# Kernel optimization log

Hardware: AMD Instinct MI355X
Metric: run time of the kernel (lower is better)

Reference implementation:

```python
import jax, jax.numpy as jnp
import numpy as np

N, D, H, L, T, R = 50000, 128, 8, 2, 4, 8
E = 800000
HD = D // H  # head_size = 16
SQRT_D = float(np.sqrt(HD))


def typed_linear(x, types, W):
    # x: (n, Din), types: (n,), W: (T, Din, Dout)  -- per-type dense projection
    out = jnp.zeros((x.shape[0], W.shape[-1]), x.dtype)
    for t in range(W.shape[0]):
        out = out + jnp.where((types == t)[:, None], x @ W[t], 0.0)
    return out


def rel_typed(x, etype, W):
    # x: (E, H, d), etype: (E,), W: (H, R, d, d) -- per-head, per-edge-type linear
    out = jnp.zeros_like(x)
    for r in range(W.shape[1]):
        out = out + jnp.where((etype == r)[:, None, None], jnp.einsum('ehd,hdo->eho', x, W[:, r]), 0.0)
    return out


def edge_softmax(a, dst, n):
    # softmax over incoming edges per destination node, per head. a: (E, H)
    amax = jax.ops.segment_max(a, dst, num_segments=n)
    amax = jnp.where(jnp.isfinite(amax), amax, 0.0)
    ex = jnp.exp(a - amax[dst])
    s = jax.ops.segment_sum(ex, dst, num_segments=n)
    return ex / (s[dst] + 1e-9)


def layer_norm(x, g, b, eps=1e-5):
    mu = x.mean(-1, keepdims=True)
    var = ((x - mu) ** 2).mean(-1, keepdims=True)
    return (x - mu) * jax.lax.rsqrt(var + eps) * g + b


def hgt_conv(x, ntype, etype, src, dst, Wk, Wq, Wv, Wa, ratt, rmsg, rpri, skip):
    n = x.shape[0]
    k = typed_linear(x, ntype, Wk).reshape(n, H, HD)
    q = typed_linear(x, ntype, Wq).reshape(n, H, HD)
    v = typed_linear(x, ntype, Wv).reshape(n, H, HD)
    kw = rel_typed(k[src], etype, ratt)               # (E, H, d)
    pri = rpri[:, etype].T                            # (E, H)
    a = (kw * q[dst]).sum(-1) * pri / SQRT_D          # (E, H)
    m = rel_typed(v[src], etype, rmsg)                # (E, H, d)
    att = edge_softmax(a, dst, n)                     # (E, H)
    h = jax.ops.segment_sum(m * att[..., None], dst, num_segments=n)
    h = h.reshape(n, D)
    h = typed_linear(h, ntype, Wa)                    # dropout off (eval)
    alpha = jax.nn.sigmoid(skip[ntype])[:, None]
    return h * alpha + x * (1.0 - alpha)


def setup_inputs() -> dict:
    key = jax.random.key(0)
    ks = jax.random.split(key, 12)
    g_lin = float(np.sqrt(2.0 / (D + D)))   # xavier-ish scale for D x D
    g_rel = float(np.sqrt(2.0 / (HD + HD)))
    g_emb = float(np.sqrt(2.0 / (N + D)))
    return {
        'embed': jax.random.normal(ks[0], (T, N, D), jnp.float32) * g_emb,
        'Wk': jax.random.normal(ks[1], (L, T, D, D), jnp.float32) * g_lin,
        'Wq': jax.random.normal(ks[2], (L, T, D, D), jnp.float32) * g_lin,
        'Wv': jax.random.normal(ks[3], (L, T, D, D), jnp.float32) * g_lin,
        'Wa': jax.random.normal(ks[4], (L, T, D, D), jnp.float32) * g_lin,
        'rel_att': jax.random.normal(ks[5], (L, H, R, HD, HD), jnp.float32) * g_rel,
        'rel_msg': jax.random.normal(ks[6], (L, H, R, HD, HD), jnp.float32) * g_rel,
        'rel_pri': jnp.ones((L, H, R), jnp.float32),
        'skip': jnp.ones((L, T), jnp.float32),
        'ln_g': jnp.ones((L, D), jnp.float32),
        'ln_b': jnp.zeros((L, D), jnp.float32),
        'src': jax.random.randint(ks[7], (E,), 0, N, jnp.int32),
        'dst': jax.random.randint(ks[8], (E,), 0, N, jnp.int32),
        'ntype': jax.random.randint(ks[9], (N,), 0, T, jnp.int32),
        'etype': jax.random.randint(ks[10], (E,), 0, R, jnp.int32),
    }


def reference(embed, Wk, Wq, Wv, Wa, rel_att, rel_msg, rel_pri, skip, ln_g, ln_b, src, dst, ntype, etype):
    # masked per-type embedding init: node gets row <rank-within-its-type> of its type table
    onehot = jax.nn.one_hot(ntype, T, dtype=jnp.int32)
    rank = jnp.take_along_axis(jnp.cumsum(onehot, axis=0), ntype[:, None], axis=1)[:, 0] - 1
    h = embed[ntype, rank]                            # (N, D)
    for l in range(L):
        h_prev = h
        hc = hgt_conv(h, ntype, etype, src, dst,
                      Wk[l], Wq[l], Wv[l], Wa[l],
                      rel_att[l], rel_msg[l], rel_pri[l], skip[l])
        h = layer_norm(hc, ln_g[l], ln_b[l]) + h_prev
    return h
```

## Files before the change

kernel.cpp:

```cpp
#include <hip/hip_runtime.h>
#include <math.h>

#define N_NODES 50000
#define DIM     128
#define NHEAD   8
#define HDIM    16
#define NLAYER  2
#define NTYPE   4
#define NREL    8
#define NEDGE   800000
#define RB      256
#define GN      8
#define NK      (N_NODES * NREL)

__device__ __forceinline__ float blo(unsigned w) { return __uint_as_float(w << 16); }
__device__ __forceinline__ float bhi(unsigned w) { return __uint_as_float(w & 0xFFFF0000u); }
__device__ __forceinline__ unsigned short f2bf(float f) {
    unsigned b = __float_as_uint(f);
    b += 0x7FFFu + ((b >> 16) & 1u);
    return (unsigned short)(b >> 16);
}


__global__ void k_hist(const int* __restrict__ ntype, int* __restrict__ hist, int n) {
    __shared__ int cnt[NTYPE];
    if (threadIdx.x < NTYPE) cnt[threadIdx.x] = 0;
    __syncthreads();
    int i = blockIdx.x * RB + threadIdx.x;
    if (i < n) atomicAdd(&cnt[ntype[i]], 1);
    __syncthreads();
    if (threadIdx.x < NTYPE) hist[blockIdx.x * NTYPE + threadIdx.x] = cnt[threadIdx.x];
}

__global__ void k_prefix(const int* __restrict__ hist, int* __restrict__ off, int nb) {
    int t = threadIdx.x;
    if (t >= NTYPE) return;
    int acc = 0;
    for (int b = 0; b < nb; b++) { off[b * NTYPE + t] = acc; acc += hist[b * NTYPE + t]; }
}

__global__ void k_rank(const int* __restrict__ ntype, const int* __restrict__ off,
                       int* __restrict__ rank, int n) {
    __shared__ int ty[RB];
    int i = blockIdx.x * RB + threadIdx.x;
    int t = (i < n) ? ntype[i] : -1;
    ty[threadIdx.x] = t;
    __syncthreads();
    if (i < n) {
        int c = 0;
        for (int j = 0; j < (int)threadIdx.x; j++) c += (ty[j] == t);
        rank[i] = off[blockIdx.x * NTYPE + t] + c;
    }
}

__global__ void k_embed(const float* __restrict__ embed, const int* __restrict__ ntype,
                        const int* __restrict__ rank, float* __restrict__ h) {
    int i = blockIdx.x;
    int t = ntype[i], r = rank[i];
    h[(size_t)i * DIM + threadIdx.x] = embed[((size_t)t * N_NODES + r) * DIM + threadIdx.x];
}

__global__ void k_typeoff(const int* __restrict__ hist, const int* __restrict__ boff,
                          int nb, int* __restrict__ typeoff) {
    if (threadIdx.x == 0 && blockIdx.x == 0) {
        int acc = 0;
        for (int t = 0; t < NTYPE; t++) {
            typeoff[t] = acc;
            acc += boff[(nb - 1) * NTYPE + t] + hist[(nb - 1) * NTYPE + t];
        }
    }
}

__global__ void k_perm(const int* __restrict__ ntype, const int* __restrict__ rank,
                       const int* __restrict__ typeoff, int* __restrict__ perm, int n) {
    int i = blockIdx.x * 256 + threadIdx.x;
    if (i < n) perm[typeoff[ntype[i]] + rank[i]] = i;
}


__global__ void k_deg2(const int* __restrict__ dst, const int* __restrict__ etype,
                       int* __restrict__ deg) {
    int e = blockIdx.x * 256 + threadIdx.x;
    if (e < NEDGE) atomicAdd(&deg[dst[e] * NREL + etype[e]], 1);
}

__global__ void k_scan1(const int* __restrict__ deg, int* __restrict__ rs,
                        int* __restrict__ bsum, int n) {
    __shared__ int sh[256];
    int i = blockIdx.x * 256 + threadIdx.x;
    int v = (i < n) ? deg[i] : 0;
    sh[threadIdx.x] = v;
    __syncthreads();
    for (int off = 1; off < 256; off <<= 1) {
        int x = (threadIdx.x >= off) ? sh[threadIdx.x - off] : 0;
        __syncthreads();
        sh[threadIdx.x] += x;
        __syncthreads();
    }
    if (i < n) rs[i] = sh[threadIdx.x] - v;
    if (threadIdx.x == 255) bsum[blockIdx.x] = sh[255];
}

__global__ void k_scan2b(int* __restrict__ bsum, int nb) {
    __shared__ int sh[256];
    __shared__ int carry;
    if (threadIdx.x == 0) carry = 0;
    __syncthreads();
    for (int base = 0; base < nb; base += 256) {
        int i = base + threadIdx.x;
        int v = (i < nb) ? bsum[i] : 0;
        sh[threadIdx.x] = v;
        __syncthreads();
        for (int off = 1; off < 256; off <<= 1) {
            int x = (threadIdx.x >= off) ? sh[threadIdx.x - off] : 0;
            __syncthreads();
            sh[threadIdx.x] += x;
            __syncthreads();
        }
        if (i < nb) bsum[i] = sh[threadIdx.x] - v + carry;
        __syncthreads();
        if (threadIdx.x == 0) carry += sh[255];
        __syncthreads();
    }
}

__global__ void k_scan3(int* __restrict__ rs, const int* __restrict__ bsum, int n) {
    int i = blockIdx.x * 256 + threadIdx.x;
    if (i < n) rs[i] += bsum[blockIdx.x];
    if (i == 0) rs[n] = NEDGE;
}

__global__ void k_scatter2(const int* __restrict__ src, const int* __restrict__ dst,
                           const int* __restrict__ etype, const int* __restrict__ rs,
                           int* __restrict__ cur, int* __restrict__ epk) {
    int e = blockIdx.x * 256 + threadIdx.x;
    if (e < NEDGE) {
        int et = etype[e];
        int key = dst[e] * NREL + et;
        int p = atomicAdd(&cur[key], 1);
        epk[rs[key] + p] = src[e] | (et << 24);
    }
}


__global__ void k_rmsgT(const float* __restrict__ rmsg, float* __restrict__ rmsgT) {
    int b = blockIdx.x;
    int d = threadIdx.x >> 4, o = threadIdx.x & 15;
    rmsgT[b * 256 + o * 16 + d] = rmsg[b * 256 + d * 16 + o];
}

__global__ void k_rattB(const float* __restrict__ ratt, unsigned short* __restrict__ rattB) {
    int i = blockIdx.x * 256 + threadIdx.x;
    rattB[i] = f2bf(ratt[i]);
}


__global__ __launch_bounds__(128) void k_qkvvt_g(
        const float* __restrict__ h, const int* __restrict__ perm, const int* __restrict__ ntype,
        const float* __restrict__ Wk, const float* __restrict__ Wq, const float* __restrict__ Wv,
        const float* __restrict__ rmsgT,
        unsigned short* __restrict__ kb, float* __restrict__ qout,
        unsigned short* __restrict__ vt, int n) {
    int o = threadIdx.x;
    int base = blockIdx.x * GN;
    __shared__ float xs[GN][DIM];
    __shared__ int nodes[GN];
    __shared__ int types[GN];
    if (o < GN) {
        int idx = base + o;
        int nd = (idx < n) ? perm[idx] : -1;
        nodes[o] = nd;
        types[o] = (nd >= 0) ? ntype[nd] : -1;
    }
    __syncthreads();
    #pragma unroll
    for (int nn = 0; nn < GN; nn++)
        if (nodes[nn] >= 0) xs[nn][o] = h[(size_t)nodes[nn] * DIM + o];
    __syncthreads();
    bool same = (nodes[GN - 1] >= 0) && (types[0] == types[GN - 1]);
    float av[GN];
    if (same) {
        int t = types[0];
        const float* wk = Wk + (size_t)t * DIM * DIM;
        const float* wq = Wq + (size_t)t * DIM * DIM;
        const float* wv = Wv + (size_t)t * DIM * DIM;
        float ak[GN], aq[GN];
        #pragma unroll
        for (int nn = 0; nn < GN; nn++) { ak[nn] = 0.f; aq[nn] = 0.f; av[nn] = 0.f; }
        for (int d = 0; d < DIM; d++) {
            float wkv = wk[d * DIM + o], wqv = wq[d * DIM + o], wvv = wv[d * DIM + o];
            #pragma unroll
            for (int nn = 0; nn < GN; nn++) {
                float xv = xs[nn][d];
                ak[nn] = fmaf(xv, wkv, ak[nn]);
                aq[nn] = fmaf(xv, wqv, aq[nn]);
                av[nn] = fmaf(xv, wvv, av[nn]);
            }
        }
        #pragma unroll
        for (int nn = 0; nn < GN; nn++) {
            size_t p = (size_t)nodes[nn] * DIM + o;
            kb[p] = f2bf(ak[nn]); qout[p] = aq[nn];
        }
    } else {
        #pragma unroll 1
        for (int nn = 0; nn < GN; nn++) {
            av[nn] = 0.f;
            if (nodes[nn] < 0) continue;
            int t = types[nn];
            const float* wk = Wk + (size_t)t * DIM * DIM;
            const float* wq = Wq + (size_t)t * DIM * DIM;
            const float* wv = Wv + (size_t)t * DIM * DIM;
            float ak = 0.f, aq = 0.f, avv = 0.f;
            for (int d = 0; d < DIM; d++) {
                float xv = xs[nn][d];
                ak = fmaf(xv, wk[d * DIM + o], ak);
                aq = fmaf(xv, wq[d * DIM + o], aq);
                avv = fmaf(xv, wv[d * DIM + o], avv);
            }
            size_t p = (size_t)nodes[nn] * DIM + o;
            kb[p] = f2bf(ak); qout[p] = aq;
            av[nn] = avv;
        }
    }
    __syncthreads();
    #pragma unroll
    for (int nn = 0; nn < GN; nn++) xs[nn][o] = av[nn];
    __syncthreads();
    int hh = o >> 4, oo = o & 15;
    #pragma unroll 1
    for (int et = 0; et < NREL; et++) {
        const float4* w4 = (const float4*)(rmsgT + ((size_t)(hh * NREL + et) * HDIM + oo) * HDIM);
        float4 w0 = w4[0], w1 = w4[1], w2 = w4[2], w3 = w4[3];
        #pragma unroll
        for (int nn = 0; nn < GN; nn++) {
            if (nodes[nn] < 0) continue;
            const float4* v4 = (const float4*)&xs[nn][hh * HDIM];
            float4 v0 = v4[0], v1 = v4[1], v2 = v4[2], v3 = v4[3];
            float acc = v0.x*w0.x + v0.y*w0.y + v0.z*w0.z + v0.w*w0.w
                      + v1.x*w1.x + v1.y*w1.y + v1.z*w1.z + v1.w*w1.w
                      + v2.x*w2.x + v2.y*w2.y + v2.z*w2.z + v2.w*w2.w
                      + v3.x*w3.x + v3.y*w3.y + v3.z*w3.z + v3.w*w3.w;
            vt[((size_t)nodes[nn] * NREL + et) * DIM + o] = f2bf(acc);
        }
    }
}


__global__ __launch_bounds__(128) void k_fused10(
        const unsigned short* __restrict__ kb, const float* __restrict__ qbuf,
        const unsigned short* __restrict__ vt,
        const int* __restrict__ rs2, const int* __restrict__ epk,
        const unsigned short* __restrict__ rattB, const float* __restrict__ rpri,
        float* __restrict__ agg) {
    int node = blockIdx.x;
    int tid = threadIdx.x;
    int hh = tid >> 4, oo = tid & 15;
    int wv = tid >> 6;
    int hl = hh & 3;

    __shared__ float q_s[DIM];
    __shared__ float u_s[NREL][NHEAD * HDIM + 4];
    __shared__ float a_sw[2][4][HDIM + 1];
    __shared__ int   es_sw[2][HDIM];

    int e0 = rs2[node * NREL];
    int e1 = rs2[node * NREL + NREL];
    if (e0 == e1) { agg[(size_t)node * DIM + tid] = 0.f; return; }

    q_s[tid] = qbuf[(size_t)node * DIM + tid];
    {
        const float4* q4 = (const float4*)&q_s[hh * HDIM];
        float4 q0 = q4[0], q1 = q4[1], q2 = q4[2], q3 = q4[3];
        #pragma unroll
        for (int et = 0; et < NREL; et++) {
            const uint4* wB = (const uint4*)(rattB + ((size_t)(hh * NREL + et) * HDIM + oo) * HDIM);
            uint4 wa = wB[0], wb = wB[1];
            float s = blo(wa.x)*q0.x + bhi(wa.x)*q0.y + blo(wa.y)*q0.z + bhi(wa.y)*q0.w
                    + blo(wa.z)*q1.x + bhi(wa.z)*q1.y + blo(wa.w)*q1.z + bhi(wa.w)*q1.w
                    + blo(wb.x)*q2.x + bhi(wb.x)*q2.y + blo(wb.y)*q2.z + bhi(wb.y)*q2.w
                    + blo(wb.z)*q3.x + bhi(wb.z)*q3.y + blo(wb.w)*q3.z + bhi(wb.w)*q3.w;
            u_s[et][tid] = s * rpri[hh * NREL + et] * 0.25f;
        }
    }

    float m_h = -1e30f, s_h = 0.f, out = 0.f;

    for (int w0e = e0; w0e < e1; w0e += HDIM) {
        int cnt = min(HDIM, e1 - w0e);
        float a = -1e30f;
        int pk = 0;
        if (oo < cnt) {
            pk = epk[w0e + oo];
            int sv = pk & 0x00FFFFFF;
            int et = ((unsigned)pk) >> 24;
            const uint4* kr = (const uint4*)(kb + (size_t)sv * DIM + hh * HDIM);
            uint4 ka = kr[0], kc = kr[1];
            const float4* u4 = (const float4*)&u_s[et][hh * HDIM];
            float4 u0 = u4[0], u1 = u4[1], u2 = u4[2], u3 = u4[3];
            a = blo(ka.x)*u0.x + bhi(ka.x)*u0.y + blo(ka.y)*u0.z + bhi(ka.y)*u0.w
              + blo(ka.z)*u1.x + bhi(ka.z)*u1.y + blo(ka.w)*u1.z + bhi(ka.w)*u1.w
              + blo(kc.x)*u2.x + bhi(kc.x)*u2.y + blo(kc.y)*u2.z + bhi(kc.y)*u2.w
              + blo(kc.z)*u3.x + bhi(kc.z)*u3.y + blo(kc.w)*u3.z + bhi(kc.w)*u3.w;
        }
        if (hl == 0) es_sw[wv][oo] = pk;
        float cmax = a;
        cmax = fmaxf(cmax, __shfl_xor(cmax, 1));
        cmax = fmaxf(cmax, __shfl_xor(cmax, 2));
        cmax = fmaxf(cmax, __shfl_xor(cmax, 4));
        cmax = fmaxf(cmax, __shfl_xor(cmax, 8));
        float m_t = (cmax > m_h + 12.f) ? cmax : m_h;
        float r = __expf(m_h - m_t);
        s_h *= r; out *= r; m_h = m_t;
        float p = (oo < cnt) ? __expf(a - m_h) : 0.f;
        float ps = p;
        ps += __shfl_xor(ps, 1);
        ps += __shfl_xor(ps, 2);
        ps += __shfl_xor(ps, 4);
        ps += __shfl_xor(ps, 8);
        s_h += ps;
        a_sw[wv][hl][oo] = p;
        for (int c = 0; c < cnt; c++) {
            float pc = a_sw[wv][hl][c];
            int pkc = es_sw[wv][c];
            int sv = pkc & 0x00FFFFFF;
            int et = ((unsigned)pkc) >> 24;
            unsigned short uv = vt[((size_t)sv * NREL + et) * DIM + tid];
            out = fmaf(pc, __uint_as_float((unsigned)uv << 16), out);
        }
    }

    agg[(size_t)node * DIM + tid] = out / (s_h + 1e-9f);
}


__global__ __launch_bounds__(128) void k_out_g(
        const float* __restrict__ agg, float* __restrict__ h,
        const int* __restrict__ perm, const int* __restrict__ ntype,
        const float* __restrict__ Wa, const float* __restrict__ skip,
        const float* __restrict__ ln_g, const float* __restrict__ ln_b, int n) {
    int o = threadIdx.x;
    int base = blockIdx.x * GN;
    __shared__ float xs[GN][DIM];
    __shared__ float hcs[GN][DIM + 1];
    __shared__ int nodes[GN];
    __shared__ int types[GN];
    __shared__ float mu_s[GN], rs_s[GN];
    if (o < GN) {
        int idx = base + o;
        int nd = (idx < n) ? perm[idx] : -1;
        nodes[o] = nd;
        types[o] = (nd >= 0) ? ntype[nd] : -1;
    }
    __syncthreads();
    #pragma unroll
    for (int nn = 0; nn < GN; nn++)
        if (nodes[nn] >= 0) xs[nn][o] = agg[(size_t)nodes[nn] * DIM + o];
    __syncthreads();
    bool same = (nodes[GN - 1] >= 0) && (types[0] == types[GN - 1]);
    if (same) {
        int t = types[0];
        const float* w = Wa + (size_t)t * DIM * DIM;
        float acc[GN];
        #pragma unroll
        for (int nn = 0; nn < GN; nn++) acc[nn] = 0.f;
        for (int d = 0; d < DIM; d++) {
            float wv = w[d * DIM + o];
            #pragma unroll
            for (int nn = 0; nn < GN; nn++) acc[nn] = fmaf(xs[nn][d], wv, acc[nn]);
        }
        float alpha = 1.f / (1.f + __expf(-skip[t]));
        #pragma unroll
        for (int nn = 0; nn < GN; nn++) {
            float hp = h[(size_t)nodes[nn] * DIM + o];
            hcs[nn][o] = acc[nn] * alpha + hp * (1.f - alpha);
        }
    } else {
        #pragma unroll 1
        for (int nn = 0; nn < GN; nn++) {
            if (nodes[nn] < 0) continue;
            int t = types[nn];
            const float* w = Wa + (size_t)t * DIM * DIM;
            float a0 = 0.f;
            for (int d = 0; d < DIM; d++) a0 = fmaf(xs[nn][d], w[d * DIM + o], a0);
            float alpha = 1.f / (1.f + __expf(-skip[t]));
            float hp = h[(size_t)nodes[nn] * DIM + o];
            hcs[nn][o] = a0 * alpha + hp * (1.f - alpha);
        }
    }
    __syncthreads();
    {
        int g = o >> 4, j = o & 15;
        if (nodes[g] >= 0) {
            float s = 0.f;
            for (int d = j; d < DIM; d += 16) s += hcs[g][d];
            #pragma unroll
            for (int m = 1; m < 16; m <<= 1) s += __shfl_xor(s, m);
            float mu = s * (1.f / DIM);
            float v = 0.f;
            for (int d = j; d < DIM; d += 16) { float dv = hcs[g][d] - mu; v = fmaf(dv, dv, v); }
            #pragma unroll
            for (int m = 1; m < 16; m <<= 1) v += __shfl_xor(v, m);
            if (j == 0) { mu_s[g] = mu; rs_s[g] = rsqrtf(v * (1.f / DIM) + 1e-5f); }
        }
    }
    __syncthreads();
    float g_o = ln_g[o], b_o = ln_b[o];
    #pragma unroll
    for (int nn = 0; nn < GN; nn++) {
        if (nodes[nn] >= 0) {
            float hp = h[(size_t)nodes[nn] * DIM + o];
            h[(size_t)nodes[nn] * DIM + o] = (hcs[nn][o] - mu_s[nn]) * rs_s[nn] * g_o + b_o + hp;
        }
    }
}


extern "C" void kernel_launch(void* const* d_in, const int* in_sizes, int n_in,
                              void* d_out, int out_size, void* d_ws, size_t ws_size,
                              hipStream_t stream) {
    const float* embed = (const float*)d_in[0];
    const float* Wk    = (const float*)d_in[1];
    const float* Wq    = (const float*)d_in[2];
    const float* Wv    = (const float*)d_in[3];
    const float* Wa    = (const float*)d_in[4];
    const float* ratt  = (const float*)d_in[5];
    const float* rmsg  = (const float*)d_in[6];
    const float* rpri  = (const float*)d_in[7];
    const float* skip  = (const float*)d_in[8];
    const float* ln_g  = (const float*)d_in[9];
    const float* ln_b  = (const float*)d_in[10];
    const int*   src   = (const int*)d_in[11];
    const int*   dst   = (const int*)d_in[12];
    const int*   ntype = (const int*)d_in[13];
    const int*   etype = (const int*)d_in[14];

    float* h = (float*)d_out;

    const size_t ND = (size_t)N_NODES * DIM;
    const int nb = (N_NODES + RB - 1) / RB;
    unsigned short* kb = (unsigned short*)d_ws;
    float* qbuf = (float*)(kb + ND);
    int* rs2  = (int*)(qbuf + ND);
    int* deg2 = rs2 + (NK + 1);
    int* cur2 = deg2 + NK;
    int* epk  = cur2 + NK;
    int* bsum = epk + NEDGE;
    int* rank = bsum + 2048;
    int* hist = rank + N_NODES;
    int* boff = hist + nb * NTYPE;
    int* typeoff = boff + nb * NTYPE;
    int* perm = typeoff + NTYPE;
    float* rmsgT = (float*)(perm + N_NODES);
    unsigned short* rattB = (unsigned short*)(rmsgT + (size_t)NLAYER * NHEAD * NREL * 256);
    unsigned short* vt = rattB + (size_t)NLAYER * NHEAD * NREL * 256;
    float* agg = qbuf;

    const int EB = (NEDGE + 255) / 256;
    const int nb2 = (NK + 255) / 256;

    k_hist<<<nb, RB, 0, stream>>>(ntype, hist, N_NODES);
    k_prefix<<<1, 64, 0, stream>>>(hist, boff, nb);
    k_rank<<<nb, RB, 0, stream>>>(ntype, boff, rank, N_NODES);
    k_embed<<<N_NODES, DIM, 0, stream>>>(embed, ntype, rank, h);
    k_typeoff<<<1, 64, 0, stream>>>(hist, boff, nb, typeoff);
    k_perm<<<nb, 256, 0, stream>>>(ntype, rank, typeoff, perm, N_NODES);

    hipMemsetAsync(deg2, 0, (size_t)NK * sizeof(int), stream);
    hipMemsetAsync(cur2, 0, (size_t)NK * sizeof(int), stream);
    k_deg2<<<EB, 256, 0, stream>>>(dst, etype, deg2);
    k_scan1<<<nb2, 256, 0, stream>>>(deg2, rs2, bsum, NK);
    k_scan2b<<<1, 256, 0, stream>>>(bsum, nb2);
    k_scan3<<<nb2, 256, 0, stream>>>(rs2, bsum, NK);
    k_scatter2<<<EB, 256, 0, stream>>>(src, dst, etype, rs2, cur2, epk);

    k_rmsgT<<<NLAYER * NHEAD * NREL, 256, 0, stream>>>(rmsg, rmsgT);
    k_rattB<<<NLAYER * NHEAD * NREL, 256, 0, stream>>>(ratt, rattB);

    const int NGB = N_NODES / GN;

    for (int l = 0; l < NLAYER; l++) {
        const float* Wk_l = Wk + (size_t)l * NTYPE * DIM * DIM;
        const float* Wq_l = Wq + (size_t)l * NTYPE * DIM * DIM;
        const float* Wv_l = Wv + (size_t)l * NTYPE * DIM * DIM;
        const float* Wa_l = Wa + (size_t)l * NTYPE * DIM * DIM;
        const unsigned short* rattB_l = rattB + (size_t)l * NHEAD * NREL * 256;
        const float* rmsgT_l = rmsgT + (size_t)l * NHEAD * NREL * 256;
        const float* rpri_l = rpri + (size_t)l * NHEAD * NREL;
        const float* skip_l = skip + (size_t)l * NTYPE;
        const float* g_l = ln_g + (size_t)l * DIM;
        const float* b_l = ln_b + (size_t)l * DIM;

        k_qkvvt_g<<<NGB, 128, 0, stream>>>(h, perm, ntype, Wk_l, Wq_l, Wv_l, rmsgT_l,
                                           kb, qbuf, vt, N_NODES);
        k_fused10<<<N_NODES, 128, 0, stream>>>(kb, qbuf, vt, rs2, epk,
                                               rattB_l, rpri_l, agg);
        k_out_g<<<NGB, 128, 0, stream>>>(agg, h, perm, ntype, Wa_l, skip_l, g_l, b_l, N_NODES);
    }
}
```

Baseline: 749.7 us.

## Compute typed QKV projections with bf16 MFMA on 32-node tiles

Replaces the scalar FP32 QKV projection kernel with one using bf16 MFMA 16x16x32 instructions over 32-node tiles of same-type nodes. The K, Q and V weights are pre-packed once into a bf16 fragment layout. Activations are converted to bf16 on load, which lowers precision of q and v. Mixed-type tiles fall back to a scalar path, and the V relation transform stays in FP32 from shared memory.

```diff
diff --git a/kernel.cpp b/kernel.cpp
--- a/kernel.cpp
+++ b/kernel.cpp
@@ -11,7 +11,11 @@
 #define NEDGE   800000
 #define RB      256
 #define GN      8
+#define MT      32
 #define NK      (N_NODES * NREL)
+
+typedef __attribute__((ext_vector_type(8))) short bf16x8;
+typedef __attribute__((ext_vector_type(4))) float f32x4;
 
 __device__ __forceinline__ float blo(unsigned w) { return __uint_as_float(w << 16); }
 __device__ __forceinline__ float bhi(unsigned w) { return __uint_as_float(w & 0xFFFF0000u); }
@@ -19,6 +23,14 @@
     unsigned b = __float_as_uint(f);
     b += 0x7FFFu + ((b >> 16) & 1u);
     return (unsigned short)(b >> 16);
+}
+__device__ __forceinline__ bf16x8 pack8(float4 x0, float4 x1) {
+    bf16x8 r;
+    r[0] = (short)f2bf(x0.x); r[1] = (short)f2bf(x0.y);
+    r[2] = (short)f2bf(x0.z); r[3] = (short)f2bf(x0.w);
+    r[4] = (short)f2bf(x1.x); r[5] = (short)f2bf(x1.y);
+    r[6] = (short)f2bf(x1.z); r[7] = (short)f2bf(x1.w);
+    return r;
 }
 
 
@@ -154,94 +166,134 @@
     rattB[i] = f2bf(ratt[i]);
 }
 
-
-__global__ __launch_bounds__(128) void k_qkvvt_g(
+__global__ void k_packW(const float* __restrict__ W, unsigned short* __restrict__ WB) {
+    int t = blockIdx.x;
+    const float* w = W + (size_t)t * 16384;
+    unsigned short* ob = WB + (size_t)t * 16384;
+    for (int idx = threadIdx.x; idx < 16384; idx += 256) {
+        int ct = idx >> 11, kc = (idx >> 9) & 3, l = (idx >> 3) & 63, j = idx & 7;
+        int k = kc * 32 + ((l >> 4) << 3) + j;
+        int c = ct * 16 + (l & 15);
+        ob[idx] = f2bf(w[k * 128 + c]);
+    }
+}
+
+
+__global__ __launch_bounds__(256) void k_qkv_mfma(
         const float* __restrict__ h, const int* __restrict__ perm, const int* __restrict__ ntype,
         const float* __restrict__ Wk, const float* __restrict__ Wq, const float* __restrict__ Wv,
-        const float* __restrict__ rmsgT,
+        const unsigned short* __restrict__ WkB, const unsigned short* __restrict__ WqB,
+        const unsigned short* __restrict__ WvB, const float* __restrict__ rmsgT,
         unsigned short* __restrict__ kb, float* __restrict__ qout,
         unsigned short* __restrict__ vt, int n) {
-    int o = threadIdx.x;
-    int base = blockIdx.x * GN;
-    __shared__ float xs[GN][DIM];
-    __shared__ int nodes[GN];
-    __shared__ int types[GN];
-    if (o < GN) {
-        int idx = base + o;
+    int tid = threadIdx.x;
+    int base = blockIdx.x * MT;
+    __shared__ int nodes_s[MT];
+    __shared__ int types_s[MT];
+    __shared__ float vs[MT][132];
+
+    if (tid < MT) {
+        int idx = base + tid;
         int nd = (idx < n) ? perm[idx] : -1;
-        nodes[o] = nd;
-        types[o] = (nd >= 0) ? ntype[nd] : -1;
-    }
-    __syncthreads();
-    #pragma unroll
-    for (int nn = 0; nn < GN; nn++)
-        if (nodes[nn] >= 0) xs[nn][o] = h[(size_t)nodes[nn] * DIM + o];
-    __syncthreads();
-    bool same = (nodes[GN - 1] >= 0) && (types[0] == types[GN - 1]);
-    float av[GN];
+        nodes_s[tid] = nd;
+        types_s[tid] = (nd >= 0) ? ntype[nd] : -1;
+    }
+    __syncthreads();
+    bool same = (nodes_s[MT - 1] >= 0) && (types_s[0] == types_s[MT - 1]);
+
     if (same) {
-        int t = types[0];
-        const float* wk = Wk + (size_t)t * DIM * DIM;
-        const float* wq = Wq + (size_t)t * DIM * DIM;
-        const float* wv = Wv + (size_t)t * DIM * DIM;
-        float ak[GN], aq[GN];
+        int l = tid & 63, w = tid >> 6;
+        int t = types_s[0];
+        const unsigned short* wbk = WkB + (size_t)t * 16384;
+        const unsigned short* wbq = WqB + (size_t)t * 16384;
+        const unsigned short* wbv = WvB + (size_t)t * 16384;
+        f32x4 acc[3][2][2];
         #pragma unroll
-        for (int nn = 0; nn < GN; nn++) { ak[nn] = 0.f; aq[nn] = 0.f; av[nn] = 0.f; }
-        for (int d = 0; d < DIM; d++) {
-            float wkv = wk[d * DIM + o], wqv = wq[d * DIM + o], wvv = wv[d * DIM + o];
+        for (int m = 0; m < 3; m++)
             #pragma unroll
-            for (int nn = 0; nn < GN; nn++) {
-                float xv = xs[nn][d];
-                ak[nn] = fmaf(xv, wkv, ak[nn]);
-                aq[nn] = fmaf(xv, wqv, aq[nn]);
-                av[nn] = fmaf(xv, wvv, av[nn]);
+            for (int a = 0; a < 2; a++)
+                #pragma unroll
+                for (int b = 0; b < 2; b++) {
+                    acc[m][a][b][0] = 0.f; acc[m][a][b][1] = 0.f;
+                    acc[m][a][b][2] = 0.f; acc[m][a][b][3] = 0.f;
+                }
+        #pragma unroll 1
+        for (int kc = 0; kc < 4; kc++) {
+            int koff = kc * 32 + ((l >> 4) << 3);
+            int r0 = l & 15;
+            const float4* p0 = (const float4*)(h + (size_t)nodes_s[r0] * DIM + koff);
+            bf16x8 a0 = pack8(p0[0], p0[1]);
+            const float4* p1 = (const float4*)(h + (size_t)nodes_s[16 + r0] * DIM + koff);
+            bf16x8 a1 = pack8(p1[0], p1[1]);
+            #pragma unroll
+            for (int cti = 0; cti < 2; cti++) {
+                int boff = ((w * 2 + cti) * 4 + kc) * 512 + l * 8;
+                bf16x8 bk = *(const bf16x8*)(wbk + boff);
+                acc[0][0][cti] = __builtin_amdgcn_mfma_f32_16x16x32_bf16(a0, bk, acc[0][0][cti], 0, 0, 0);
+                acc[0][1][cti] = __builtin_amdgcn_mfma_f32_16x16x32_bf16(a1, bk, acc[0][1][cti], 0, 0, 0);
+                bf16x8 bq = *(const bf16x8*)(wbq + boff);
+                acc[1][0][cti] = __builtin_amdgcn_mfma_f32_16x16x32_bf16(a0, bq, acc[1][0][cti], 0, 0, 0);
+                acc[1][1][cti] = __builtin_amdgcn_mfma_f32_16x16x32_bf16(a1, bq, acc[1][1][cti], 0, 0, 0);
+                bf16x8 bv = *(const bf16x8*)(wbv + boff);
+                acc[2][0][cti] = __builtin_amdgcn_mfma_f32_16x16x32_bf16(a0, bv, acc[2][0][cti], 0, 0, 0);
+                acc[2][1][cti] = __builtin_amdgcn_mfma_f32_16x16x32_bf16(a1, bv, acc[2][1][cti], 0, 0, 0);
             }
         }
         #pragma unroll
-        for (int nn = 0; nn < GN; nn++) {
-            size_t p = (size_t)nodes[nn] * DIM + o;
-            kb[p] = f2bf(ak[nn]); qout[p] = aq[nn];
-        }
+        for (int mt = 0; mt < 2; mt++)
+            #pragma unroll
+            for (int cti = 0; cti < 2; cti++) {
+                int col = w * 32 + cti * 16 + (l & 15);
+                #pragma unroll
+                for (int r = 0; r < 4; r++) {
+                    int row = mt * 16 + ((l >> 4) << 2) + r;
+                    size_t p = (size_t)nodes_s[row] * DIM + col;
+                    kb[p] = f2bf(acc[0][mt][cti][r]);
+                    qout[p] = acc[1][mt][cti][r];
+                    vs[row][col] = acc[2][mt][cti][r];
+                }
+            }
     } else {
-        #pragma unroll 1
-        for (int nn = 0; nn < GN; nn++) {
-            av[nn] = 0.f;
-            if (nodes[nn] < 0) continue;
-            int t = types[nn];
-            const float* wk = Wk + (size_t)t * DIM * DIM;
-            const float* wq = Wq + (size_t)t * DIM * DIM;
-            const float* wv = Wv + (size_t)t * DIM * DIM;
-            float ak = 0.f, aq = 0.f, avv = 0.f;
+        int o = tid & 127, half = tid >> 7;
+        for (int nn = half; nn < MT; nn += 2) {
+            int nd = nodes_s[nn];
+            if (nd < 0) continue;
+            int t = types_s[nn];
+            const float* wk = Wk + (size_t)t * 16384;
+            const float* wq = Wq + (size_t)t * 16384;
+            const float* wv = Wv + (size_t)t * 16384;
+            float ak = 0.f, aq = 0.f, av = 0.f;
             for (int d = 0; d < DIM; d++) {
-                float xv = xs[nn][d];
+                float xv = h[(size_t)nd * DIM + d];
                 ak = fmaf(xv, wk[d * DIM + o], ak);
                 aq = fmaf(xv, wq[d * DIM + o], aq);
-                avv = fmaf(xv, wv[d * DIM + o], avv);
+                av = fmaf(xv, wv[d * DIM + o], av);
             }
-            size_t p = (size_t)nodes[nn] * DIM + o;
+            size_t p = (size_t)nd * DIM + o;
             kb[p] = f2bf(ak); qout[p] = aq;
-            av[nn] = avv;
-        }
-    }
-    __syncthreads();
-    #pragma unroll
-    for (int nn = 0; nn < GN; nn++) xs[nn][o] = av[nn];
-    __syncthreads();
-    int hh = o >> 4, oo = o & 15;
-    #pragma unroll 1
-    for (int et = 0; et < NREL; et++) {
-        const float4* w4 = (const float4*)(rmsgT + ((size_t)(hh * NREL + et) * HDIM + oo) * HDIM);
-        float4 w0 = w4[0], w1 = w4[1], w2 = w4[2], w3 = w4[3];
-        #pragma unroll
-        for (int nn = 0; nn < GN; nn++) {
-            if (nodes[nn] < 0) continue;
-            const float4* v4 = (const float4*)&xs[nn][hh * HDIM];
-            float4 v0 = v4[0], v1 = v4[1], v2 = v4[2], v3 = v4[3];
-            float acc = v0.x*w0.x + v0.y*w0.y + v0.z*w0.z + v0.w*w0.w
-                      + v1.x*w1.x + v1.y*w1.y + v1.z*w1.z + v1.w*w1.w
-                      + v2.x*w2.x + v2.y*w2.y + v2.z*w2.z + v2.w*w2.w
-                      + v3.x*w3.x + v3.y*w3.y + v3.z*w3.z + v3.w*w3.w;
-            vt[((size_t)nodes[nn] * NREL + et) * DIM + o] = f2bf(acc);
+            vs[nn][o] = av;
+        }
+    }
+    __syncthreads();
+    {
+        int o = tid & 127, half = tid >> 7;
+        int hh = o >> 4, oo = o & 15;
+        #pragma unroll 1
+        for (int et = 0; et < NREL; et++) {
+            const float4* w4 = (const float4*)(rmsgT + ((size_t)(hh * NREL + et) * HDIM + oo) * HDIM);
+            float4 w0 = w4[0], w1 = w4[1], w2 = w4[2], w3 = w4[3];
+            for (int i = 0; i < 16; i++) {
+                int nn = half * 16 + i;
+                int nd = nodes_s[nn];
+                if (nd < 0) continue;
+                const float4* v4 = (const float4*)&vs[nn][hh * HDIM];
+                float4 v0 = v4[0], v1 = v4[1], v2 = v4[2], v3 = v4[3];
+                float a2 = v0.x*w0.x + v0.y*w0.y + v0.z*w0.z + v0.w*w0.w
+                         + v1.x*w1.x + v1.y*w1.y + v1.z*w1.z + v1.w*w1.w
+                         + v2.x*w2.x + v2.y*w2.y + v2.z*w2.z + v2.w*w2.w
+                         + v3.x*w3.x + v3.y*w3.y + v3.z*w3.z + v3.w*w3.w;
+                vt[((size_t)nd * NREL + et) * DIM + o] = f2bf(a2);
+            }
         }
     }
 }
@@ -454,6 +506,7 @@
     float* rmsgT = (float*)(perm + N_NODES);
     unsigned short* rattB = (unsigned short*)(rmsgT + (size_t)NLAYER * NHEAD * NREL * 256);
     unsigned short* vt = rattB + (size_t)NLAYER * NHEAD * NREL * 256;
+    unsigned short* wpk = vt + (size_t)N_NODES * NREL * DIM;
     float* agg = qbuf;
 
     const int EB = (NEDGE + 255) / 256;
@@ -476,14 +529,26 @@
 
     k_rmsgT<<<NLAYER * NHEAD * NREL, 256, 0, stream>>>(rmsg, rmsgT);
     k_rattB<<<NLAYER * NHEAD * NREL, 256, 0, stream>>>(ratt, rattB);
+    for (int l = 0; l < NLAYER; l++) {
+        k_packW<<<NTYPE, 256, 0, stream>>>(Wk + (size_t)l * NTYPE * 16384,
+                                           wpk + ((size_t)l * 3 + 0) * NTYPE * 16384);
+        k_packW<<<NTYPE, 256, 0, stream>>>(Wq + (size_t)l * NTYPE * 16384,
+                                           wpk + ((size_t)l * 3 + 1) * NTYPE * 16384);
+        k_packW<<<NTYPE, 256, 0, stream>>>(Wv + (size_t)l * NTYPE * 16384,
+                                           wpk + ((size_t)l * 3 + 2) * NTYPE * 16384);
+    }
 
     const int NGB = N_NODES / GN;
+    const int NMB = (N_NODES + MT - 1) / MT;
 
     for (int l = 0; l < NLAYER; l++) {
         const float* Wk_l = Wk + (size_t)l * NTYPE * DIM * DIM;
         const float* Wq_l = Wq + (size_t)l * NTYPE * DIM * DIM;
         const float* Wv_l = Wv + (size_t)l * NTYPE * DIM * DIM;
         const float* Wa_l = Wa + (size_t)l * NTYPE * DIM * DIM;
+        const unsigned short* wkB_l = wpk + ((size_t)l * 3 + 0) * NTYPE * 16384;
+        const unsigned short* wqB_l = wpk + ((size_t)l * 3 + 1) * NTYPE * 16384;
+        const unsigned short* wvB_l = wpk + ((size_t)l * 3 + 2) * NTYPE * 16384;
         const unsigned short* rattB_l = rattB + (size_t)l * NHEAD * NREL * 256;
         const float* rmsgT_l = rmsgT + (size_t)l * NHEAD * NREL * 256;
         const float* rpri_l = rpri + (size_t)l * NHEAD * NREL;
@@ -491,8 +556,9 @@
         const float* g_l = ln_g + (size_t)l * DIM;
         const float* b_l = ln_b + (size_t)l * DIM;
 
-        k_qkvvt_g<<<NGB, 128, 0, stream>>>(h, perm, ntype, Wk_l, Wq_l, Wv_l, rmsgT_l,
-                                           kb, qbuf, vt, N_NODES);
+        k_qkv_mfma<<<NMB, 256, 0, stream>>>(h, perm, ntype, Wk_l, Wq_l, Wv_l,
+                                            wkB_l, wqB_l, wvB_l, rmsgT_l,
+                                            kb, qbuf, vt, N_NODES);
         k_fused10<<<N_NODES, 128, 0, stream>>>(kb, qbuf, vt, rs2, epk,
                                                rattB_l, rpri_l, agg);
         k_out_g<<<NGB, 128, 0, stream>>>(agg, h, perm, ntype, Wa_l, skip_l, g_l, b_l, N_NODES);
```

Result: slower. 808.1 us (+7.8%).
